# Performance work log

Hardware: AMD Instinct MI355X
Metric: run time of the kernel (lower is better)

The kernel has to match this reference:

```python
import jax, jax.numpy as jnp
import numpy as np

H = 2048   # hidden_size
K = 2048   # key_size
Q = 2048   # query_size
S = 8192   # source sequence length
V = 2048   # value feature dim


def setup_inputs() -> dict:
    key = jax.random.key(0)
    ks = jax.random.split(key, 6)
    query = jax.random.normal(ks[0], (1, 1, Q), dtype=jnp.float32)
    src_key = jax.random.normal(ks[1], (1, S, K), dtype=jnp.float32)
    values = jax.random.normal(ks[2], (S, V), dtype=jnp.float32)
    # nn.Linear weights are [out, in]; all bias-free
    Wq = jax.random.normal(ks[3], (H, Q), dtype=jnp.float32) / np.sqrt(Q)
    Wk = jax.random.normal(ks[4], (H, K), dtype=jnp.float32) / np.sqrt(K)
    Ws = jax.random.normal(ks[5], (1, H), dtype=jnp.float32) / np.sqrt(H)
    return {"query": query, "key": src_key, "values": values,
            "Wq": Wq, "Wk": Wk, "Ws": Ws}


def reference(query, key, values, Wq, Wk, Ws):
    # projected_query: [1,1,H]; projected_key: [1,S,H]
    pq = jnp.einsum('btq,hq->bth', query, Wq)
    pk = jnp.einsum('bsk,hk->bsh', key, Wk)
    # additive (Bahdanau) scores: [1,S,1] -> squeeze(2).unsqueeze(1) -> [1,1,S]
    scores = jnp.einsum('bsh,oh->bso', jnp.tanh(pq + pk), Ws)
    scores = scores[:, :, 0][:, None, :]
    attention_weights = jax.nn.softmax(scores, axis=-1)        # [1,1,S]
    # bmm([1,1,S], values.unsqueeze(0)=[1,S,V]) -> [1,1,V]
    context = jnp.einsum('bts,sv->btv', attention_weights, values)
    return (attention_weights, context)
```

## Files before the change

kernel.cpp:

```cpp
#include <hip/hip_runtime.h>
#include <hip/hip_bf16.h>
#include <math.h>

#define HDIM 2048
#define KDIM 2048
#define SDIM 8192
#define VDIM 2048
#define BKT  64
#define NT   (KDIM / BKT)

using short8 = __attribute__((ext_vector_type(8))) short;
using f32x4  = __attribute__((ext_vector_type(4))) float;
using us8    = __attribute__((ext_vector_type(8))) unsigned short;

typedef const __attribute__((address_space(1))) void g_void;
typedef __attribute__((address_space(3))) void lds_void;

__device__ __forceinline__ unsigned short f2bf(float f) {
  union { float f; unsigned int u; } x; x.f = f;
  unsigned int r = x.u + 0x7fffu + ((x.u >> 16) & 1u);
  return (unsigned short)(r >> 16);
}

__device__ __forceinline__ float tanh_fast(float x) {
  float e = __expf(2.0f * x);
  return 1.0f - 2.0f * __builtin_amdgcn_rcpf(e + 1.0f);
}

__device__ __forceinline__ void barrier_sync() {
  asm volatile("" ::: "memory");
  __builtin_amdgcn_s_barrier();
  asm volatile("" ::: "memory");
}

__global__ __launch_bounds__(256) void cvt_pq_kernel(const float* __restrict__ key,
                                                     const float* __restrict__ Wk,
                                                     unsigned short* __restrict__ outbf,
                                                     const float* __restrict__ query,
                                                     const float* __restrict__ Wq,
                                                     float* __restrict__ pq,
                                                     int keyN8, int cvtBlocks) {
  if ((int)blockIdx.x < cvtBlocks) {
    int i = blockIdx.x * 256 + threadIdx.x;
    const float* src = (i < keyN8) ? &key[(size_t)i * 8] : &Wk[((size_t)i - keyN8) * 8];
    f32x4 a = *(const f32x4*)src;
    f32x4 b = *(const f32x4*)(src + 4);
    us8 o;
    #pragma unroll
    for (int j = 0; j < 4; ++j) { o[j] = f2bf(a[j]); o[j + 4] = f2bf(b[j]); }
    *(us8*)&outbf[(size_t)i * 8] = o;
  } else {
    int wave = threadIdx.x >> 6, lane = threadIdx.x & 63;
    int h = (blockIdx.x - cvtBlocks) * 4 + wave;
    const float* w = Wq + (size_t)h * KDIM;
    f32x4 s4 = (f32x4)(0.0f);
    #pragma unroll
    for (int i = 0; i < KDIM / 256; ++i) {
      f32x4 q4 = *(const f32x4*)&query[lane * 4 + i * 256];
      f32x4 w4 = *(const f32x4*)&w[lane * 4 + i * 256];
      #pragma unroll
      for (int j = 0; j < 4; ++j) s4[j] = fmaf(q4[j], w4[j], s4[j]);
    }
    float s = s4[0] + s4[1] + s4[2] + s4[3];
    #pragma unroll
    for (int off = 32; off; off >>= 1) s += __shfl_xor(s, off);
    if (lane == 0) pq[h] = s;
  }
}

__global__ __launch_bounds__(512, 2) void scores_kernel(const unsigned short* __restrict__ keybf,
                                                        const unsigned short* __restrict__ wkbf,
                                                        const float* __restrict__ pq,
                                                        const float* __restrict__ Ws,
                                                        float* __restrict__ partial) {
  __shared__ unsigned short lds[65536];

  const int tid = threadIdx.x;
  const int bid = blockIdx.x;
  const int xg = bid & 7, xi = bid >> 3;
  const int bx = xg * 4 + (xi & 3);
  const int by = xi >> 2;
  const int s0 = bx * 256, h0 = by * 256;

  const int wave = tid >> 6, lane = tid & 63;
  const int wm = wave >> 2, wn = wave & 3;
  const int l16 = lane & 15, g16 = lane >> 4;

  const int srow = tid >> 3;
  const int scol = ((tid & 7) * 16) ^ ((srow & 7) << 4);
  const char* aSrc0 = (const char*)keybf + ((size_t)(s0 + srow) * KDIM) * 2 + scol;
  const char* bSrc0 = (const char*)wkbf  + ((size_t)(h0 + srow) * KDIM) * 2 + scol;

  #define STAGE_A(o, kt, buf) __builtin_amdgcn_global_load_lds( \
      (g_void*)(aSrc0 + (size_t)(o) * 64 * KDIM * 2 + (size_t)(kt) * 128), \
      (lds_void*)((char*)lds + (size_t)(buf) * 65536 + (o) * 8192 + wave * 1024), 16, 0, 0)
  #define STAGE_B(o, kt, buf) __builtin_amdgcn_global_load_lds( \
      (g_void*)(bSrc0 + (size_t)(o) * 64 * KDIM * 2 + (size_t)(kt) * 128), \
      (lds_void*)((char*)lds + (size_t)(buf) * 65536 + 32768 + (o) * 8192 + wave * 1024), 16, 0, 0)

  const int xorv = (l16 & 7) << 4;
  int colx[2];
  colx[0] = ((g16 * 16)      ) ^ xorv;
  colx[1] = ((g16 * 16) | 64 ) ^ xorv;
  const int aRowBase = (wm * 128 + l16) * 128;
  const int bRowBase = 32768 + (wn * 64 + l16) * 128;

  f32x4 acc[8][4];
  #pragma unroll
  for (int m = 0; m < 8; ++m)
    #pragma unroll
    for (int n = 0; n < 4; ++n) acc[m][n] = (f32x4)(0.0f);

  STAGE_A(0, 0, 0); STAGE_A(2, 0, 0);
  STAGE_B(0, 0, 0); STAGE_B(1, 0, 0); STAGE_B(2, 0, 0); STAGE_B(3, 0, 0);
  STAGE_A(1, 0, 0); STAGE_A(3, 0, 0);
  asm volatile("s_waitcnt vmcnt(2)" ::: "memory");
  barrier_sync();

  short8 af[4][2], bf_[4][2];

  for (int t = 0; t < NT; ++t) {
    const int cbase = (t & 1) * 65536;
    const int nbuf = (t & 1) ^ 1;
    const bool more = (t + 1 < NT);

    #pragma unroll
    for (int m = 0; m < 4; ++m)
      #pragma unroll
      for (int ks = 0; ks < 2; ++ks)
        af[m][ks] = *(const short8*)((const char*)lds + cbase + aRowBase + m * 2048 + colx[ks]);
    #pragma unroll
    for (int n = 0; n < 2; ++n)
      #pragma unroll
      for (int ks = 0; ks < 2; ++ks)
        bf_[n][ks] = *(const short8*)((const char*)lds + cbase + bRowBase + n * 2048 + colx[ks]);
    if (more) {
      STAGE_A(0, t + 1, nbuf); STAGE_A(2, t + 1, nbuf);
      STAGE_B(0, t + 1, nbuf); STAGE_B(1, t + 1, nbuf);
    }
    barrier_sync();
    __builtin_amdgcn_s_setprio(1);
    #pragma unroll
    for (int m = 0; m < 4; ++m)
      #pragma unroll
      for (int n = 0; n < 2; ++n)
        #pragma unroll
        for (int ks = 0; ks < 2; ++ks)
          acc[m][n] = __builtin_amdgcn_mfma_f32_16x16x32_bf16(af[m][ks], bf_[n][ks], acc[m][n], 0, 0, 0);
    __builtin_amdgcn_s_setprio(0);
    barrier_sync();

    #pragma unroll
    for (int n = 2; n < 4; ++n)
      #pragma unroll
      for (int ks = 0; ks < 2; ++ks)
        bf_[n][ks] = *(const short8*)((const char*)lds + cbase + bRowBase + n * 2048 + colx[ks]);
    if (more) {
      STAGE_B(2, t + 1, nbuf); STAGE_B(3, t + 1, nbuf);
      STAGE_A(1, t + 1, nbuf); STAGE_A(3, t + 1, nbuf);
    }
    barrier_sync();
    __builtin_amdgcn_s_setprio(1);
    #pragma unroll
    for (int m = 0; m < 4; ++m)
      #pragma unroll
      for (int n = 2; n < 4; ++n)
        #pragma unroll
        for (int ks = 0; ks < 2; ++ks)
          acc[m][n] = __builtin_amdgcn_mfma_f32_16x16x32_bf16(af[m][ks], bf_[n][ks], acc[m][n], 0, 0, 0);
    __builtin_amdgcn_s_setprio(0);
    if (more)
      asm volatile("s_waitcnt vmcnt(8)" ::: "memory");
    else
      asm volatile("s_waitcnt vmcnt(0)" ::: "memory");
    barrier_sync();

    #pragma unroll
    for (int m = 0; m < 4; ++m)
      #pragma unroll
      for (int ks = 0; ks < 2; ++ks)
        af[m][ks] = *(const short8*)((const char*)lds + cbase + aRowBase + (m + 4) * 2048 + colx[ks]);
    barrier_sync();
    __builtin_amdgcn_s_setprio(1);
    #pragma unroll
    for (int m = 0; m < 4; ++m)
      #pragma unroll
      for (int n = 2; n < 4; ++n)
        #pragma unroll
        for (int ks = 0; ks < 2; ++ks)
          acc[m + 4][n] = __builtin_amdgcn_mfma_f32_16x16x32_bf16(af[m][ks], bf_[n][ks], acc[m + 4][n], 0, 0, 0);
    __builtin_amdgcn_s_setprio(0);
    barrier_sync();

    __builtin_amdgcn_s_setprio(1);
    #pragma unroll
    for (int m = 0; m < 4; ++m)
      #pragma unroll
      for (int n = 0; n < 2; ++n)
        #pragma unroll
        for (int ks = 0; ks < 2; ++ks)
          acc[m + 4][n] = __builtin_amdgcn_mfma_f32_16x16x32_bf16(af[m][ks], bf_[n][ks], acc[m + 4][n], 0, 0, 0);
    __builtin_amdgcn_s_setprio(0);
    if (more)
      asm volatile("s_waitcnt vmcnt(2)" ::: "memory");
    else
      asm volatile("s_waitcnt vmcnt(0)" ::: "memory");
    barrier_sync();
  }

  float pqv[4], wsv[4];
  #pragma unroll
  for (int n = 0; n < 4; ++n) {
    int h = h0 + wn * 64 + n * 16 + l16;
    pqv[n] = pq[h];
    wsv[n] = Ws[h];
  }

  float* sred = (float*)lds;
  #pragma unroll
  for (int m = 0; m < 8; ++m) {
    #pragma unroll
    for (int j = 0; j < 4; ++j) {
      float rs = 0.f;
      #pragma unroll
      for (int n = 0; n < 4; ++n)
        rs += tanh_fast(acc[m][n][j] + pqv[n]) * wsv[n];
      rs += __shfl_xor(rs, 1);
      rs += __shfl_xor(rs, 2);
      rs += __shfl_xor(rs, 4);
      rs += __shfl_xor(rs, 8);
      if (l16 == 0)
        sred[(wm * 128 + m * 16 + g16 * 4 + j) * 4 + wn] = rs;
    }
  }
  __syncthreads();
  if (tid < 256) {
    float v = sred[tid * 4 + 0] + sred[tid * 4 + 1] + sred[tid * 4 + 2] + sred[tid * 4 + 3];
    partial[(size_t)(s0 + tid) * 8 + by] = v;
  }
}

__global__ __launch_bounds__(1024) void softmax_kernel(const float* __restrict__ partial,
                                                       float* __restrict__ weights) {
  __shared__ float red[16];
  int tid = threadIdx.x;
  int sbase = tid * 8;
  float sc[8];
  float mx = -1e30f;
  #pragma unroll
  for (int i = 0; i < 8; ++i) {
    const float* p = partial + (size_t)(sbase + i) * 8;
    float v = 0.f;
    #pragma unroll
    for (int q = 0; q < 8; ++q) v += p[q];
    sc[i] = v;
    mx = fmaxf(mx, v);
  }
  #pragma unroll
  for (int off = 32; off; off >>= 1) mx = fmaxf(mx, __shfl_xor(mx, off));
  if ((tid & 63) == 0) red[tid >> 6] = mx;
  __syncthreads();
  float gmx = red[0];
  #pragma unroll
  for (int q = 1; q < 16; ++q) gmx = fmaxf(gmx, red[q]);
  __syncthreads();
  float ls = 0.f;
  #pragma unroll
  for (int i = 0; i < 8; ++i) { sc[i] = expf(sc[i] - gmx); ls += sc[i]; }
  #pragma unroll
  for (int off = 32; off; off >>= 1) ls += __shfl_xor(ls, off);
  if ((tid & 63) == 0) red[tid >> 6] = ls;
  __syncthreads();
  float gs = 0.f;
  #pragma unroll
  for (int q = 0; q < 16; ++q) gs += red[q];
  float inv = 1.0f / gs;
  #pragma unroll
  for (int i = 0; i < 8; ++i) weights[sbase + i] = sc[i] * inv;
}

__global__ __launch_bounds__(256) void ctx_partial_kernel(const float* __restrict__ values,
                                                          const float* __restrict__ w,
                                                          float* __restrict__ part) {
  int vcol4 = blockIdx.x * 256 + threadIdx.x;
  int ss0 = blockIdx.y * 64;
  f32x4 acc = (f32x4)(0.0f);
  for (int s = ss0; s < ss0 + 64; ++s) {
    f32x4 v = *(const f32x4*)&values[(size_t)s * VDIM + vcol4 * 4];
    float ws = w[s];
    #pragma unroll
    for (int j = 0; j < 4; ++j) acc[j] = fmaf(ws, v[j], acc[j]);
  }
  *(f32x4*)&part[(size_t)blockIdx.y * VDIM + vcol4 * 4] = acc;
}

__global__ __launch_bounds__(256) void ctx_reduce_kernel(const float* __restrict__ part,
                                                         float* __restrict__ ctx) {
  int vcol = blockIdx.x * 256 + threadIdx.x;
  float acc = 0.f;
  #pragma unroll
  for (int p = 0; p < 128; ++p) acc += part[(size_t)p * VDIM + vcol];
  ctx[vcol] = acc;
}

extern "C" void kernel_launch(void* const* d_in, const int* in_sizes, int n_in,
                              void* d_out, int out_size, void* d_ws, size_t ws_size,
                              hipStream_t stream) {
  const float* query  = (const float*)d_in[0];
  const float* key    = (const float*)d_in[1];
  const float* values = (const float*)d_in[2];
  const float* Wq     = (const float*)d_in[3];
  const float* Wk     = (const float*)d_in[4];
  const float* Ws     = (const float*)d_in[5];

  float* out     = (float*)d_out;
  float* weights = out;
  float* ctx     = out + SDIM;

  char* ws = (char*)d_ws;
  unsigned short* keybf = (unsigned short*)ws;
  unsigned short* wkbf  = (unsigned short*)(ws + (size_t)SDIM * KDIM * 2);
  char* tail = ws + (size_t)SDIM * KDIM * 2 + (size_t)HDIM * KDIM * 2;
  float* pq      = (float*)tail;
  float* partial = (float*)(tail + 8192);
  float* cpart   = (float*)(tail + 8192 + (size_t)SDIM * 8 * 4);

  const int keyN8 = SDIM * KDIM / 8;
  const int totN8 = keyN8 + HDIM * KDIM / 8;
  const int cvtBlocks = totN8 / 256;
  cvt_pq_kernel<<<cvtBlocks + HDIM / 4, 256, 0, stream>>>(key, Wk, keybf, query, Wq, pq,
                                                          keyN8, cvtBlocks);
  scores_kernel<<<256, 512, 0, stream>>>(keybf, wkbf, pq, Ws, partial);
  softmax_kernel<<<1, 1024, 0, stream>>>(partial, weights);
  ctx_partial_kernel<<<dim3(VDIM / (256 * 4), 128), 256, 0, stream>>>(values, weights, cpart);
  ctx_reduce_kernel<<<VDIM / 256, 256, 0, stream>>>(cpart, ctx);
}
```

Measured before the change: 138.7 us.

## Collapse the split ping-pong main loop into one-barrier-per-tile double buffering

Replaces the four-phase per-tile schedule, which interleaved partial LDS fragment loads, staged global-to-LDS copies and MFMA groups separated by several barriers, with a simpler loop. The new loop loads all B fragments and half the A fragments, issues every prefetch for the next tile, runs all MFMAs, then loads the other A half and waits with vmcnt(0) behind a single barrier. This cuts barrier overhead and lets more MFMAs run back to back. In exchange it loses the staggered interleaving of loads with compute and keeps more fragments live in registers, which may lower overlap or occupancy.

```diff
diff --git a/kernel.cpp b/kernel.cpp
--- a/kernel.cpp
+++ b/kernel.cpp
@@ -111,10 +111,9 @@
     #pragma unroll
     for (int n = 0; n < 4; ++n) acc[m][n] = (f32x4)(0.0f);
 
-  STAGE_A(0, 0, 0); STAGE_A(2, 0, 0);
+  STAGE_A(0, 0, 0); STAGE_A(1, 0, 0); STAGE_A(2, 0, 0); STAGE_A(3, 0, 0);
   STAGE_B(0, 0, 0); STAGE_B(1, 0, 0); STAGE_B(2, 0, 0); STAGE_B(3, 0, 0);
-  STAGE_A(1, 0, 0); STAGE_A(3, 0, 0);
-  asm volatile("s_waitcnt vmcnt(2)" ::: "memory");
+  asm volatile("s_waitcnt vmcnt(0)" ::: "memory");
   barrier_sync();
 
   short8 af[4][2], bf_[4][2];
@@ -130,81 +129,45 @@
       for (int ks = 0; ks < 2; ++ks)
         af[m][ks] = *(const short8*)((const char*)lds + cbase + aRowBase + m * 2048 + colx[ks]);
     #pragma unroll
-    for (int n = 0; n < 2; ++n)
+    for (int n = 0; n < 4; ++n)
       #pragma unroll
       for (int ks = 0; ks < 2; ++ks)
         bf_[n][ks] = *(const short8*)((const char*)lds + cbase + bRowBase + n * 2048 + colx[ks]);
+
     if (more) {
-      STAGE_A(0, t + 1, nbuf); STAGE_A(2, t + 1, nbuf);
+      STAGE_A(0, t + 1, nbuf); STAGE_A(1, t + 1, nbuf);
+      STAGE_A(2, t + 1, nbuf); STAGE_A(3, t + 1, nbuf);
       STAGE_B(0, t + 1, nbuf); STAGE_B(1, t + 1, nbuf);
+      STAGE_B(2, t + 1, nbuf); STAGE_B(3, t + 1, nbuf);
     }
-    barrier_sync();
+
     __builtin_amdgcn_s_setprio(1);
     #pragma unroll
-    for (int m = 0; m < 4; ++m)
-      #pragma unroll
-      for (int n = 0; n < 2; ++n)
+    for (int ks = 0; ks < 2; ++ks)
+      #pragma unroll
+      for (int m = 0; m < 4; ++m)
         #pragma unroll
-        for (int ks = 0; ks < 2; ++ks)
+        for (int n = 0; n < 4; ++n)
           acc[m][n] = __builtin_amdgcn_mfma_f32_16x16x32_bf16(af[m][ks], bf_[n][ks], acc[m][n], 0, 0, 0);
     __builtin_amdgcn_s_setprio(0);
-    barrier_sync();
-
-    #pragma unroll
-    for (int n = 2; n < 4; ++n)
-      #pragma unroll
-      for (int ks = 0; ks < 2; ++ks)
-        bf_[n][ks] = *(const short8*)((const char*)lds + cbase + bRowBase + n * 2048 + colx[ks]);
-    if (more) {
-      STAGE_B(2, t + 1, nbuf); STAGE_B(3, t + 1, nbuf);
-      STAGE_A(1, t + 1, nbuf); STAGE_A(3, t + 1, nbuf);
-    }
-    barrier_sync();
-    __builtin_amdgcn_s_setprio(1);
-    #pragma unroll
-    for (int m = 0; m < 4; ++m)
-      #pragma unroll
-      for (int n = 2; n < 4; ++n)
-        #pragma unroll
-        for (int ks = 0; ks < 2; ++ks)
-          acc[m][n] = __builtin_amdgcn_mfma_f32_16x16x32_bf16(af[m][ks], bf_[n][ks], acc[m][n], 0, 0, 0);
-    __builtin_amdgcn_s_setprio(0);
-    if (more)
-      asm volatile("s_waitcnt vmcnt(8)" ::: "memory");
-    else
-      asm volatile("s_waitcnt vmcnt(0)" ::: "memory");
-    barrier_sync();
 
     #pragma unroll
     for (int m = 0; m < 4; ++m)
       #pragma unroll
       for (int ks = 0; ks < 2; ++ks)
         af[m][ks] = *(const short8*)((const char*)lds + cbase + aRowBase + (m + 4) * 2048 + colx[ks]);
-    barrier_sync();
+
     __builtin_amdgcn_s_setprio(1);
     #pragma unroll
-    for (int m = 0; m < 4; ++m)
-      #pragma unroll
-      for (int n = 2; n < 4; ++n)
+    for (int ks = 0; ks < 2; ++ks)
+      #pragma unroll
+      for (int m = 0; m < 4; ++m)
         #pragma unroll
-        for (int ks = 0; ks < 2; ++ks)
+        for (int n = 0; n < 4; ++n)
           acc[m + 4][n] = __builtin_amdgcn_mfma_f32_16x16x32_bf16(af[m][ks], bf_[n][ks], acc[m + 4][n], 0, 0, 0);
     __builtin_amdgcn_s_setprio(0);
-    barrier_sync();
-
-    __builtin_amdgcn_s_setprio(1);
-    #pragma unroll
-    for (int m = 0; m < 4; ++m)
-      #pragma unroll
-      for (int n = 0; n < 2; ++n)
-        #pragma unroll
-        for (int ks = 0; ks < 2; ++ks)
-          acc[m + 4][n] = __builtin_amdgcn_mfma_f32_16x16x32_bf16(af[m][ks], bf_[n][ks], acc[m + 4][n], 0, 0, 0);
-    __builtin_amdgcn_s_setprio(0);
-    if (more)
-      asm volatile("s_waitcnt vmcnt(2)" ::: "memory");
-    else
-      asm volatile("s_waitcnt vmcnt(0)" ::: "memory");
+
+    asm volatile("s_waitcnt vmcnt(0)" ::: "memory");
     barrier_sync();
   }
 
```

Measured after the change: 136.1 us. Within noise of the previous version (-1.9%).
